# Performance work log

Measured on AMD Instinct MI355X. Metric: run time of the kernel, lower is better.

The kernel has to match this reference:

```python
import jax, jax.numpy as jnp
import numpy as np

B, T_NEW, C = 8, 128, 2048
H, T_PAST = 16, 2048
D = C // H  # head_dim = 128


def setup_inputs() -> dict:
    key = jax.random.key(0)
    ks = jax.random.split(key, 12)
    s = 0.02
    inp = {
        "x": jax.random.normal(ks[0], (B, T_NEW, C), dtype=jnp.float32),
        "K_past": jax.random.normal(ks[1], (B, H, T_PAST, D), dtype=jnp.float32),
        "V_past": jax.random.normal(ks[2], (B, H, T_PAST, D), dtype=jnp.float32),
        "Wq": jax.random.normal(ks[3], (C, C), dtype=jnp.float32) * s,
        "bq": jnp.zeros((C,), dtype=jnp.float32),
        "Wk": jax.random.normal(ks[4], (C, C), dtype=jnp.float32) * s,
        "bk": jnp.zeros((C,), dtype=jnp.float32),
        "Wv": jax.random.normal(ks[5], (C, C), dtype=jnp.float32) * s,
        "bv": jnp.zeros((C,), dtype=jnp.float32),
        "Wo": jax.random.normal(ks[6], (C, C), dtype=jnp.float32) * s,
        "bo": jnp.zeros((C,), dtype=jnp.float32),
        "position_offset": T_PAST,
    }
    return inp


def reference(x, K_past, V_past, Wq, bq, Wk, bk, Wv, bv, Wo, bo, position_offset):
    b, t_new, c = x.shape
    h = K_past.shape[1]
    d = c // h
    t_past = K_past.shape[2]

    def split_heads(t):  # (B,T,C) -> (B,H,T,D)
        return t.reshape(b, t_new, h, d).transpose(0, 2, 1, 3)

    Q = split_heads(x @ Wq + bq)
    K_new = split_heads(x @ Wk + bk)
    V_new = split_heads(x @ Wv + bv)

    K = jnp.concatenate([K_past, K_new], axis=2)  # (B,H,T_total,D)
    V = jnp.concatenate([V_past, V_new], axis=2)

    # global positions: past keys are 0..T_past-1, new keys/queries start at position_offset
    key_global = jnp.concatenate(
        [jnp.arange(t_past), position_offset + jnp.arange(t_new)]
    )
    query_global = position_offset + jnp.arange(t_new)
    causal_mask = key_global[None, :] <= query_global[:, None]  # (T_new, T_total)

    scale = 1.0 / jnp.sqrt(jnp.asarray(d, dtype=x.dtype))
    scores = jnp.einsum("bhqd,bhkd->bhqk", Q, K) * scale
    scores = jnp.where(causal_mask[None, None], scores, jnp.finfo(scores.dtype).min)
    weights = jax.nn.softmax(scores, axis=-1)

    out = jnp.einsum("bhqk,bhkd->bhqd", weights, V)
    out = out.transpose(0, 2, 1, 3).reshape(b, t_new, c)
    return out @ Wo + bo, K, V
```

## Files before the change

### kernel.cpp

```cpp
#include <hip/hip_runtime.h>
#include <hip/hip_bf16.h>

#define B_  8
#define TN_ 128
#define C_  2048
#define H_  16
#define TP_ 2048
#define D_  128
#define TT_ 2176
#define M_  1024

typedef __attribute__((ext_vector_type(8))) short bf16x8;
typedef __attribute__((ext_vector_type(4))) float f32x4;

static __device__ __forceinline__ unsigned short f2bu(float f) {
    unsigned int u = __float_as_uint(f);
    unsigned int r = (u + 0x7FFFu + ((u >> 16) & 1u)) >> 16;
    return (unsigned short)r;
}

__global__ __launch_bounds__(256) void copy_past_kernel(
    const float* __restrict__ Kp, const float* __restrict__ Vp,
    float* __restrict__ Ko, float* __restrict__ Vo)
{
    const long long NV = (long long)B_ * H_ * TP_ * D_ / 4;
    long long stride = (long long)gridDim.x * blockDim.x;
    for (long long idx = (long long)blockIdx.x * blockDim.x + threadIdx.x;
         idx < 2 * NV; idx += stride) {
        int sel = idx >= NV;
        long long v = sel ? idx - NV : idx;
        long long bh = v >> 16;
        long long r  = v & 65535;
        const float4* s = (const float4*)((sel ? Vp : Kp) + (bh << 18)) + r;
        float4* d = (float4*)((sel ? Vo : Ko) + bh * (long long)(TT_ * D_)) + r;
        *d = *s;
    }
}

__global__ __launch_bounds__(256) void gemm_kernel(
    const float* __restrict__ A,
    const float* __restrict__ W,
    const float* __restrict__ bias,
    float* __restrict__ out,
    int scatter)
{
    __shared__ float As[32][68];
    __shared__ float Bs[32][68];
    const int tid = threadIdx.x;
    const int m0 = blockIdx.y * 64, n0 = blockIdx.x * 64;
    const int ty = tid >> 4, tx = tid & 15;
    const int arow = tid >> 2, akg = (tid & 3) * 8;
    float acc[4][4] = {{0.f}};

    for (int kt = 0; kt < C_; kt += 32) {
        const float4* ap = (const float4*)(A + (long long)(m0 + arow) * C_ + kt + akg);
        float4 a0 = ap[0], a1 = ap[1];
        As[akg + 0][arow] = a0.x; As[akg + 1][arow] = a0.y;
        As[akg + 2][arow] = a0.z; As[akg + 3][arow] = a0.w;
        As[akg + 4][arow] = a1.x; As[akg + 5][arow] = a1.y;
        As[akg + 6][arow] = a1.z; As[akg + 7][arow] = a1.w;
        #pragma unroll
        for (int it = 0; it < 2; ++it) {
            int kl = (tid >> 4) + it * 16;
            *(float4*)&Bs[kl][tx * 4] =
                *(const float4*)(W + (long long)(kt + kl) * C_ + n0 + tx * 4);
        }
        __syncthreads();
        #pragma unroll
        for (int kk = 0; kk < 32; ++kk) {
            float4 a = *(const float4*)&As[kk][ty * 4];
            float4 b = *(const float4*)&Bs[kk][tx * 4];
            acc[0][0] += a.x * b.x; acc[0][1] += a.x * b.y; acc[0][2] += a.x * b.z; acc[0][3] += a.x * b.w;
            acc[1][0] += a.y * b.x; acc[1][1] += a.y * b.y; acc[1][2] += a.y * b.z; acc[1][3] += a.y * b.w;
            acc[2][0] += a.z * b.x; acc[2][1] += a.z * b.y; acc[2][2] += a.z * b.z; acc[2][3] += a.z * b.w;
            acc[3][0] += a.w * b.x; acc[3][1] += a.w * b.y; acc[3][2] += a.w * b.z; acc[3][3] += a.w * b.w;
        }
        __syncthreads();
    }
    float bb[4];
    #pragma unroll
    for (int j = 0; j < 4; ++j) bb[j] = bias[n0 + tx * 4 + j];
    #pragma unroll
    for (int i = 0; i < 4; ++i) {
        int m = m0 + ty * 4 + i;
        #pragma unroll
        for (int j = 0; j < 4; ++j) {
            int n = n0 + tx * 4 + j;
            float r = acc[i][j] + bb[j];
            if (!scatter) {
                out[(long long)m * C_ + n] = r;
            } else {
                int b2 = m >> 7, t = m & 127, h2 = n >> 7, d2 = n & 127;
                out[(((long long)(b2 * H_ + h2)) * TT_ + TP_ + t) * D_ + d2] = r;
            }
        }
    }
}

__global__ __launch_bounds__(256) void attn_mfma_kernel(
    const float* __restrict__ Qw,
    const float* __restrict__ Kf,
    const float* __restrict__ Vf,
    float* __restrict__ Ow,
    const int* __restrict__ poff)
{
    __shared__ __align__(16) unsigned short Ks[64][136];
    __shared__ __align__(16) unsigned short Vt[128][72];
    __shared__ __align__(16) unsigned short Pw[4][16][72];

    const int tid = threadIdx.x;
    const int lane = tid & 63;
    const int w = tid >> 6;
    const int lr = lane & 15;
    const int lg = lane >> 4;
    const int bh = blockIdx.x, b = bh >> 4, h = bh & 15;
    const int q0 = blockIdx.y * 64;
    const int off = *poff;
    const float scale = 0.08838834764831843f;

    bf16x8 qf[4];
    {
        const float* qsrc = Qw + ((long long)(b * TN_ + q0 + w * 16 + lr)) * C_ + h * D_;
        #pragma unroll
        for (int kt = 0; kt < 4; ++kt) {
            const float4* p4 = (const float4*)(qsrc + kt * 32 + lg * 8);
            float4 x0 = p4[0], x1 = p4[1];
            union { unsigned short u[8]; bf16x8 v; } pk;
            pk.u[0] = f2bu(x0.x); pk.u[1] = f2bu(x0.y);
            pk.u[2] = f2bu(x0.z); pk.u[3] = f2bu(x0.w);
            pk.u[4] = f2bu(x1.x); pk.u[5] = f2bu(x1.y);
            pk.u[6] = f2bu(x1.z); pk.u[7] = f2bu(x1.w);
            qf[kt] = pk.v;
        }
    }

    const int skey = tid >> 2, sdg = (tid & 3) * 32;
    const int vd = tid & 127, vhalf = tid >> 7;
    const int vswz = (vd >> 3) & 7;
    const int tq = q0 + w * 16 + lg * 4;

    float m_r[4], l_r[4];
    f32x4 ov[8];
    #pragma unroll
    for (int r = 0; r < 4; ++r) { m_r[r] = -1e30f; l_r[r] = 0.f; }
    #pragma unroll
    for (int dt = 0; dt < 8; ++dt) ov[dt] = (f32x4){0.f, 0.f, 0.f, 0.f};

    const int upper = TP_ + q0 + 64;

    for (int kc = 0; kc < upper; kc += 64) {
        __syncthreads();
        {
            const float4* ksrc = (const float4*)(Kf + ((long long)bh * TT_ + kc + skey) * D_ + sdg);
            #pragma unroll
            for (int u = 0; u < 8; ++u) {
                float4 k4 = ksrc[u];
                ushort4 kp;
                kp.x = f2bu(k4.x); kp.y = f2bu(k4.y); kp.z = f2bu(k4.z); kp.w = f2bu(k4.w);
                *(ushort4*)&Ks[skey][sdg + u * 4] = kp;
            }
        }
        {
            const float* vsrc = Vf + ((long long)bh * TT_ + kc) * D_ + vd;
            #pragma unroll
            for (int j = 0; j < 8; ++j) {
                int k4 = vhalf * 32 + j * 4;
                float a0 = vsrc[(k4 + 0) * D_];
                float a1 = vsrc[(k4 + 1) * D_];
                float a2 = vsrc[(k4 + 2) * D_];
                float a3 = vsrc[(k4 + 3) * D_];
                ushort4 vp;
                vp.x = f2bu(a0); vp.y = f2bu(a1); vp.z = f2bu(a2); vp.w = f2bu(a3);
                int col = (((k4 >> 3) ^ vswz) << 3) + (k4 & 7);
                *(ushort4*)&Vt[vd][col] = vp;
            }
        }
        __syncthreads();

        f32x4 sa[4];
        #pragma unroll
        for (int n = 0; n < 4; ++n) {
            f32x4 acc = (f32x4){0.f, 0.f, 0.f, 0.f};
            #pragma unroll
            for (int kt = 0; kt < 4; ++kt) {
                bf16x8 kfrag = *(const bf16x8*)&Ks[n * 16 + lr][kt * 32 + lg * 8];
                acc = __builtin_amdgcn_mfma_f32_16x16x32_bf16(qf[kt], kfrag, acc, 0, 0, 0);
            }
            sa[n] = acc;
        }

        float sv[4][4];
        #pragma unroll
        for (int n = 0; n < 4; ++n) {
            int kg = kc + n * 16 + lr;
            #pragma unroll
            for (int r = 0; r < 4; ++r) {
                bool okm = (kg < TP_) ? (kg <= off + tq + r) : (kg - TP_ <= tq + r);
                sv[n][r] = okm ? sa[n][r] * scale : -1e30f;
            }
        }

        #pragma unroll
        for (int r = 0; r < 4; ++r) {
            float mloc = fmaxf(fmaxf(sv[0][r], sv[1][r]), fmaxf(sv[2][r], sv[3][r]));
            #pragma unroll
            for (int dx = 1; dx < 16; dx <<= 1) mloc = fmaxf(mloc, __shfl_xor(mloc, dx));
            float mnew = fmaxf(m_r[r], mloc);
            float alpha = __expf(m_r[r] - mnew);
            float psum = 0.f;
            #pragma unroll
            for (int n = 0; n < 4; ++n) {
                float p = __expf(sv[n][r] - mnew);
                psum += p;
                Pw[w][lg * 4 + r][n * 16 + lr] = f2bu(p);
            }
            #pragma unroll
            for (int dx = 1; dx < 16; dx <<= 1) psum += __shfl_xor(psum, dx);
            m_r[r] = mnew;
            l_r[r] = l_r[r] * alpha + psum;
            #pragma unroll
            for (int dt = 0; dt < 8; ++dt) ov[dt][r] *= alpha;
        }

        bf16x8 pf0 = *(const bf16x8*)&Pw[w][lr][lg * 8];
        bf16x8 pf1 = *(const bf16x8*)&Pw[w][lr][32 + lg * 8];
        #pragma unroll
        for (int dt = 0; dt < 8; ++dt) {
            int d = dt * 16 + lr;
            int sw = (d >> 3) & 7;
            bf16x8 vf0 = *(const bf16x8*)&Vt[d][(lg ^ sw) << 3];
            ov[dt] = __builtin_amdgcn_mfma_f32_16x16x32_bf16(pf0, vf0, ov[dt], 0, 0, 0);
            bf16x8 vf1 = *(const bf16x8*)&Vt[d][((4 + lg) ^ sw) << 3];
            ov[dt] = __builtin_amdgcn_mfma_f32_16x16x32_bf16(pf1, vf1, ov[dt], 0, 0, 0);
        }
    }

    #pragma unroll
    for (int r = 0; r < 4; ++r) {
        float inv = 1.0f / l_r[r];
        float* dst = Ow + ((long long)(b * TN_ + tq + r)) * C_ + h * D_ + lr;
        #pragma unroll
        for (int dt = 0; dt < 8; ++dt) dst[dt * 16] = ov[dt][r] * inv;
    }
}

extern "C" void kernel_launch(void* const* d_in, const int* in_sizes, int n_in,
                              void* d_out, int out_size, void* d_ws, size_t ws_size,
                              hipStream_t stream)
{
    (void)in_sizes; (void)n_in; (void)out_size; (void)ws_size;
    const float* x  = (const float*)d_in[0];
    const float* Kp = (const float*)d_in[1];
    const float* Vp = (const float*)d_in[2];
    const float* Wq = (const float*)d_in[3];
    const float* bq = (const float*)d_in[4];
    const float* Wk = (const float*)d_in[5];
    const float* bk = (const float*)d_in[6];
    const float* Wv = (const float*)d_in[7];
    const float* bv = (const float*)d_in[8];
    const float* Wo = (const float*)d_in[9];
    const float* bo = (const float*)d_in[10];
    const int* poff = (const int*)d_in[11];

    float* out = (float*)d_out;
    float* Ko  = out + (long long)M_ * C_;
    float* Vo  = Ko + (long long)B_ * H_ * TT_ * D_;

    float* Qws = (float*)d_ws;
    float* Aws = Qws + (long long)M_ * C_;

    hipLaunchKernelGGL(copy_past_kernel, dim3(8192), dim3(256), 0, stream, Kp, Vp, Ko, Vo);
    dim3 gg(C_ / 64, M_ / 64);
    hipLaunchKernelGGL(gemm_kernel, gg, dim3(256), 0, stream, x, Wq, bq, Qws, 0);
    hipLaunchKernelGGL(gemm_kernel, gg, dim3(256), 0, stream, x, Wk, bk, Ko, 1);
    hipLaunchKernelGGL(gemm_kernel, gg, dim3(256), 0, stream, x, Wv, bv, Vo, 1);
    hipLaunchKernelGGL(attn_mfma_kernel, dim3(B_ * H_, TN_ / 64), dim3(256), 0, stream,
                       Qws, Ko, Vo, Aws, poff);
    hipLaunchKernelGGL(gemm_kernel, gg, dim3(256), 0, stream, Aws, Wo, bo, out, 0);
}
```

Measured before the change: 1.269 ms.

## Use split-bf16 MFMA (3-pass) for fp32 projection GEMMs

```diff
diff --git a/kernel.cpp b/kernel.cpp
--- a/kernel.cpp
+++ b/kernel.cpp
@@ -17,6 +17,13 @@
     unsigned int u = __float_as_uint(f);
     unsigned int r = (u + 0x7FFFu + ((u >> 16) & 1u)) >> 16;
     return (unsigned short)r;
+}
+
+static __device__ __forceinline__ void split2(float x, unsigned short& h, unsigned short& l) {
+    unsigned int u = __float_as_uint(x);
+    unsigned int hu = u & 0xFFFF0000u;
+    h = (unsigned short)(hu >> 16);
+    l = f2bu(x - __uint_as_float(hu));
 }
 
 __global__ __launch_bounds__(256) void copy_past_kernel(
@@ -44,54 +51,95 @@
     float* __restrict__ out,
     int scatter)
 {
-    __shared__ float As[32][68];
-    __shared__ float Bs[32][68];
+    __shared__ __align__(16) unsigned short Ah[64][72], Al[64][72];
+    __shared__ __align__(16) unsigned short Bh[128][72], Bl[128][72];
+
     const int tid = threadIdx.x;
-    const int m0 = blockIdx.y * 64, n0 = blockIdx.x * 64;
-    const int ty = tid >> 4, tx = tid & 15;
-    const int arow = tid >> 2, akg = (tid & 3) * 8;
-    float acc[4][4] = {{0.f}};
-
-    for (int kt = 0; kt < C_; kt += 32) {
-        const float4* ap = (const float4*)(A + (long long)(m0 + arow) * C_ + kt + akg);
-        float4 a0 = ap[0], a1 = ap[1];
-        As[akg + 0][arow] = a0.x; As[akg + 1][arow] = a0.y;
-        As[akg + 2][arow] = a0.z; As[akg + 3][arow] = a0.w;
-        As[akg + 4][arow] = a1.x; As[akg + 5][arow] = a1.y;
-        As[akg + 6][arow] = a1.z; As[akg + 7][arow] = a1.w;
-        #pragma unroll
-        for (int it = 0; it < 2; ++it) {
-            int kl = (tid >> 4) + it * 16;
-            *(float4*)&Bs[kl][tx * 4] =
-                *(const float4*)(W + (long long)(kt + kl) * C_ + n0 + tx * 4);
-        }
+    const int m0 = blockIdx.x * 64, n0 = blockIdx.y * 128;
+
+    const int ar = tid >> 2;
+    const int ak = (tid & 3) * 16;
+    const int bn = tid & 127;
+    const int bkh = (tid >> 7) * 32;
+
+    const int lane = tid & 63, w = tid >> 6;
+    const int lr = lane & 15, lg = lane >> 4;
+    const int wm = (w >> 1) * 32, wn = (w & 1) * 64;
+
+    f32x4 acc[2][4];
+    #pragma unroll
+    for (int i = 0; i < 2; ++i)
+        #pragma unroll
+        for (int j = 0; j < 4; ++j) acc[i][j] = (f32x4){0.f, 0.f, 0.f, 0.f};
+
+    for (int kt = 0; kt < C_; kt += 64) {
         __syncthreads();
-        #pragma unroll
-        for (int kk = 0; kk < 32; ++kk) {
-            float4 a = *(const float4*)&As[kk][ty * 4];
-            float4 b = *(const float4*)&Bs[kk][tx * 4];
-            acc[0][0] += a.x * b.x; acc[0][1] += a.x * b.y; acc[0][2] += a.x * b.z; acc[0][3] += a.x * b.w;
-            acc[1][0] += a.y * b.x; acc[1][1] += a.y * b.y; acc[1][2] += a.y * b.z; acc[1][3] += a.y * b.w;
-            acc[2][0] += a.z * b.x; acc[2][1] += a.z * b.y; acc[2][2] += a.z * b.z; acc[2][3] += a.z * b.w;
-            acc[3][0] += a.w * b.x; acc[3][1] += a.w * b.y; acc[3][2] += a.w * b.z; acc[3][3] += a.w * b.w;
+        {
+            const float4* ap = (const float4*)(A + (long long)(m0 + ar) * C_ + kt + ak);
+            #pragma unroll
+            for (int j = 0; j < 4; ++j) {
+                float4 x = ap[j];
+                ushort4 h4, l4;
+                split2(x.x, h4.x, l4.x); split2(x.y, h4.y, l4.y);
+                split2(x.z, h4.z, l4.z); split2(x.w, h4.w, l4.w);
+                *(ushort4*)&Ah[ar][ak + j * 4] = h4;
+                *(ushort4*)&Al[ar][ak + j * 4] = l4;
+            }
+        }
+        {
+            const float* wp = W + (long long)(kt + bkh) * C_ + n0 + bn;
+            #pragma unroll
+            for (int j = 0; j < 8; ++j) {
+                float x0 = wp[(j * 4 + 0) * C_];
+                float x1 = wp[(j * 4 + 1) * C_];
+                float x2 = wp[(j * 4 + 2) * C_];
+                float x3 = wp[(j * 4 + 3) * C_];
+                ushort4 h4, l4;
+                split2(x0, h4.x, l4.x); split2(x1, h4.y, l4.y);
+                split2(x2, h4.z, l4.z); split2(x3, h4.w, l4.w);
+                *(ushort4*)&Bh[bn][bkh + j * 4] = h4;
+                *(ushort4*)&Bl[bn][bkh + j * 4] = l4;
+            }
         }
         __syncthreads();
-    }
-    float bb[4];
-    #pragma unroll
-    for (int j = 0; j < 4; ++j) bb[j] = bias[n0 + tx * 4 + j];
-    #pragma unroll
-    for (int i = 0; i < 4; ++i) {
-        int m = m0 + ty * 4 + i;
-        #pragma unroll
-        for (int j = 0; j < 4; ++j) {
-            int n = n0 + tx * 4 + j;
-            float r = acc[i][j] + bb[j];
-            if (!scatter) {
-                out[(long long)m * C_ + n] = r;
-            } else {
-                int b2 = m >> 7, t = m & 127, h2 = n >> 7, d2 = n & 127;
-                out[(((long long)(b2 * H_ + h2)) * TT_ + TP_ + t) * D_ + d2] = r;
+
+        #pragma unroll
+        for (int ks = 0; ks < 2; ++ks) {
+            const int ko = ks * 32 + lg * 8;
+            bf16x8 ah0 = *(const bf16x8*)&Ah[wm + lr][ko];
+            bf16x8 ah1 = *(const bf16x8*)&Ah[wm + 16 + lr][ko];
+            bf16x8 al0 = *(const bf16x8*)&Al[wm + lr][ko];
+            bf16x8 al1 = *(const bf16x8*)&Al[wm + 16 + lr][ko];
+            #pragma unroll
+            for (int nt = 0; nt < 4; ++nt) {
+                bf16x8 bh = *(const bf16x8*)&Bh[wn + nt * 16 + lr][ko];
+                bf16x8 bl = *(const bf16x8*)&Bl[wn + nt * 16 + lr][ko];
+                acc[0][nt] = __builtin_amdgcn_mfma_f32_16x16x32_bf16(ah0, bh, acc[0][nt], 0, 0, 0);
+                acc[0][nt] = __builtin_amdgcn_mfma_f32_16x16x32_bf16(al0, bh, acc[0][nt], 0, 0, 0);
+                acc[0][nt] = __builtin_amdgcn_mfma_f32_16x16x32_bf16(ah0, bl, acc[0][nt], 0, 0, 0);
+                acc[1][nt] = __builtin_amdgcn_mfma_f32_16x16x32_bf16(ah1, bh, acc[1][nt], 0, 0, 0);
+                acc[1][nt] = __builtin_amdgcn_mfma_f32_16x16x32_bf16(al1, bh, acc[1][nt], 0, 0, 0);
+                acc[1][nt] = __builtin_amdgcn_mfma_f32_16x16x32_bf16(ah1, bl, acc[1][nt], 0, 0, 0);
+            }
+        }
+    }
+
+    #pragma unroll
+    for (int nt = 0; nt < 4; ++nt) {
+        const int n = n0 + wn + nt * 16 + lr;
+        const float bb = bias[n];
+        #pragma unroll
+        for (int mt = 0; mt < 2; ++mt) {
+            #pragma unroll
+            for (int r = 0; r < 4; ++r) {
+                const int m = m0 + wm + mt * 16 + lg * 4 + r;
+                float v = acc[mt][nt][r] + bb;
+                if (!scatter) {
+                    out[(long long)m * C_ + n] = v;
+                } else {
+                    int b2 = m >> 7, t = m & 127, h2 = n >> 7, d2 = n & 127;
+                    out[(((long long)(b2 * H_ + h2)) * TT_ + TP_ + t) * D_ + d2] = v;
+                }
             }
         }
     }
@@ -270,7 +318,7 @@
     float* Aws = Qws + (long long)M_ * C_;
 
     hipLaunchKernelGGL(copy_past_kernel, dim3(8192), dim3(256), 0, stream, Kp, Vp, Ko, Vo);
-    dim3 gg(C_ / 64, M_ / 64);
+    dim3 gg(M_ / 64, C_ / 128);
     hipLaunchKernelGGL(gemm_kernel, gg, dim3(256), 0, stream, x, Wq, bq, Qws, 0);
     hipLaunchKernelGGL(gemm_kernel, gg, dim3(256), 0, stream, x, Wk, bk, Ko, 1);
     hipLaunchKernelGGL(gemm_kernel, gg, dim3(256), 0, stream, x, Wv, bv, Vo, 1);
```

After: 1.077 ms. 1.18x faster.
